# Performance work log

Hardware: AMD Instinct MI355X
Metric: run time of the kernel (lower is better)

## Reference

```python
import jax, jax.numpy as jnp
import numpy as np

EMBED = 512
H = 8
HD = EMBED // H           # 64
NUM_CLS = 4
WIN = 32                  # one-sided window radius
DIL = 1
WLEN = 2 * WIN + 1        # 65
CTX = NUM_CLS + WLEN      # 69
PATCH_LEN = 8192
B = 1
S = NUM_CLS + PATCH_LEN
THETA = 10000.0
COORD_HIGH = 100000.0
NEG = -1e30


def _rotate_half(x):
    # [..., x1, x2, ...] -> [..., -x2, x1, ...]
    x1 = x[..., 0::2]
    x2 = x[..., 1::2]
    return jnp.stack([-x2, x1], axis=-1).reshape(x.shape)


def _rope2d(x, coords):
    # x: (B,H,L,HD), coords: (B,L,2)
    half = HD // 2
    inv_freq = 1.0 / (THETA ** (jnp.arange(0, half, 2, dtype=jnp.float32) / half))  # (half//2,)
    xy = coords / COORD_HIGH
    fx = xy[..., 0][..., None] * inv_freq   # (B,L,half//2)
    fy = xy[..., 1][..., None] * inv_freq
    fx = jnp.repeat(fx, 2, axis=-1)         # (B,L,half)
    fy = jnp.repeat(fy, 2, axis=-1)
    freqs = jnp.concatenate([fx, fy], axis=-1)[:, None]  # (B,1,L,HD)
    return x * jnp.cos(freqs) + _rotate_half(x) * jnp.sin(freqs)


def setup_inputs() -> dict:
    key = jax.random.key(0)
    k1, k2, k3, k4, k5, k6 = jax.random.split(key, 6)
    x = jax.random.normal(k1, (B, S, EMBED), dtype=jnp.float32)
    coords = jax.random.uniform(k2, (B, PATCH_LEN, 2), dtype=jnp.float32) * COORD_HIGH
    sc = 1.0 / np.sqrt(EMBED)
    w_qkv = jax.random.normal(k3, (3 * EMBED, EMBED), dtype=jnp.float32) * sc
    b_qkv = jax.random.normal(k4, (3 * EMBED,), dtype=jnp.float32) * 0.02
    w_out = jax.random.normal(k5, (EMBED, EMBED), dtype=jnp.float32) * sc
    b_out = jax.random.normal(k6, (EMBED,), dtype=jnp.float32) * 0.02
    return {"x": x, "coords": coords, "w_qkv": w_qkv, "b_qkv": b_qkv,
            "w_out": w_out, "b_out": b_out}


def _forward(x, coords, w_qkv, b_qkv, w_out, b_out):
    Bb, seq_len, _ = x.shape
    qkv = x @ w_qkv.T + b_qkv                       # (B,S,3E)
    qkv = qkv.reshape(Bb, seq_len, 3, H, HD)
    qkv = jnp.transpose(qkv, (2, 0, 3, 1, 4))       # (3,B,H,S,HD)
    q, k, v = qkv[0], qkv[1], qkv[2]
    q_cls, k_cls, v_cls = q[:, :, :NUM_CLS], k[:, :, :NUM_CLS], v[:, :, :NUM_CLS]
    q_p, k_p, v_p = q[:, :, NUM_CLS:], k[:, :, NUM_CLS:], v[:, :, NUM_CLS:]

    q_p = _rope2d(q_p, coords)
    k_p = _rope2d(k_p, coords)
    k_all = jnp.concatenate([k_cls, k_p], axis=2)
    v_all = v

    scale = 1.0 / np.sqrt(HD)

    # --- global CLS attention: CLS queries attend to everything ---
    cls_scores = jnp.einsum('bhqd,bhkd->bhqk', q_cls, k_all) * scale
    cls_probs = jax.nn.softmax(cls_scores, axis=-1)
    cls_out = jnp.einsum('bhqk,bhkd->bhqd', cls_probs, v_all)

    # --- windowed patch attention: patch i -> [CLS | patches i-W..i+W (dilated)] ---
    L = PATCH_LEN
    pad = WIN * DIL
    k_pad = jnp.pad(k_p, ((0, 0), (0, 0), (pad, pad), (0, 0)))
    v_pad = jnp.pad(v_p, ((0, 0), (0, 0), (pad, pad), (0, 0)))
    gather_idx = jnp.arange(L)[:, None] + jnp.arange(WLEN)[None, :] * DIL  # (L,WLEN)
    k_win = k_pad[:, :, gather_idx]   # (B,H,L,WLEN,HD)
    v_win = v_pad[:, :, gather_idx]

    s_cls = jnp.einsum('bhld,bhcd->bhlc', q_p, k_cls) * scale     # (B,H,L,NUM_CLS)
    s_win = jnp.einsum('bhld,bhlwd->bhlw', q_p, k_win) * scale    # (B,H,L,WLEN)

    pos = jnp.arange(L)[:, None] + (jnp.arange(WLEN)[None, :] - WIN) * DIL
    in_bounds = (pos >= 0) & (pos < L)                            # (L,WLEN)
    s_win = jnp.where(in_bounds[None, None], s_win, NEG)

    scores = jnp.concatenate([s_cls, s_win], axis=-1)             # (B,H,L,CTX)
    probs = jax.nn.softmax(scores, axis=-1)
    p_cls, p_win = probs[..., :NUM_CLS], probs[..., NUM_CLS:]
    patch_out = (jnp.einsum('bhlc,bhcd->bhld', p_cls, v_cls)
                 + jnp.einsum('bhlw,bhlwd->bhld', p_win, v_win))

    out = jnp.concatenate([cls_out, patch_out], axis=2)           # (B,H,S,HD)
    out = jnp.transpose(out, (0, 2, 1, 3)).reshape(Bb, seq_len, EMBED)
    return out @ w_out.T + b_out


def reference(x, coords, w_qkv, b_qkv, w_out, b_out):
    return _forward(x, coords, w_qkv, b_qkv, w_out, b_out)
```

## Files before the change

kernel.cpp:

```cpp
#include <hip/hip_runtime.h>
#include <math.h>

#define EMBED 512
#define NHEAD 8
#define HD 64
#define NUM_CLS 4
#define WIN 32
#define WLEN 65
#define PATCH_LEN 8192
#define S_TOT 8196
#define QKV_LD 1536
#define VT_LD 8200

typedef short bf16x8 __attribute__((ext_vector_type(8)));
typedef float f32x4 __attribute__((ext_vector_type(4)));

__device__ __forceinline__ unsigned short f2bf(float f) {
    unsigned u = __float_as_uint(f);
    return (unsigned short)((u + 0x7fffu + ((u >> 16) & 1u)) >> 16);
}
__device__ __forceinline__ float bf2f(unsigned short v) {
    return __uint_as_float((unsigned)v << 16);
}
__device__ __forceinline__ void gll16(const unsigned short* g, unsigned short* l) {
    __builtin_amdgcn_global_load_lds((const __attribute__((address_space(1))) void*)g,
                                     (__attribute__((address_space(3))) void*)l, 16, 0, 0);
}

__global__ __launch_bounds__(256) void cast_all(const float* __restrict__ x,
                                                const float* __restrict__ wq,
                                                const float* __restrict__ wo,
                                                unsigned short* __restrict__ xb,
                                                unsigned short* __restrict__ wqb,
                                                unsigned short* __restrict__ wob)
{
    const int n1 = S_TOT * EMBED;
    const int n2 = 3 * EMBED * EMBED;
    const int n3 = EMBED * EMBED;
    const int i = (blockIdx.x * 256 + threadIdx.x) * 4;
    const float* src;
    unsigned short* dst;
    int j;
    if (i < n1)           { src = x;  dst = xb;  j = i; }
    else if (i < n1 + n2) { src = wq; dst = wqb; j = i - n1; }
    else if (i < n1 + n2 + n3) { src = wo; dst = wob; j = i - n1 - n2; }
    else return;
    const float4 v = *(const float4*)(src + j);
    ushort4 o;
    o.x = f2bf(v.x); o.y = f2bf(v.y); o.z = f2bf(v.z); o.w = f2bf(v.w);
    *(ushort4*)(dst + j) = o;
}

#define EXW 136
__global__ __launch_bounds__(256) void gemm_qkv(const unsigned short* __restrict__ A,
                                                const unsigned short* __restrict__ B,
                                                const float* __restrict__ bias,
                                                unsigned short* __restrict__ C,
                                                const float* __restrict__ coords,
                                                unsigned short* __restrict__ vT)
{
    const int M = S_TOT, N = 3 * EMBED, K = EMBED;
    __shared__ __align__(16) unsigned short As[2][128 * 32];
    __shared__ __align__(16) unsigned short Bs[2][128 * 32];
    __shared__ __align__(16) unsigned short EX[64 * EXW];
    const int tid = threadIdx.x;
    const int lane = tid & 63, w = tid >> 6;
    const int bn = blockIdx.x, bm = blockIdx.y;

    const int ar0 = tid >> 2;
    const int col8 = (tid & 3) * 8;
    int gm0 = bm * 128 + ar0;       if (gm0 >= M) gm0 = M - 1;
    int gm1 = bm * 128 + ar0 + 64;  if (gm1 >= M) gm1 = M - 1;
    const unsigned short* pa0 = A + (size_t)gm0 * K + col8;
    const unsigned short* pa1 = A + (size_t)gm1 * K + col8;
    const unsigned short* pb0 = B + (size_t)(bn * 128 + ar0) * K + col8;
    const unsigned short* pb1 = B + (size_t)(bn * 128 + ar0 + 64) * K + col8;

    const int wr = (w & 1) * 64;
    const int wc = (w >> 1) * 64;
    const int fr = lane & 15;
    const int fk = (lane >> 4) * 8;

    f32x4 acc[4][4];
#pragma unroll
    for (int mi = 0; mi < 4; ++mi)
#pragma unroll
        for (int ni = 0; ni < 4; ++ni) acc[mi][ni] = (f32x4)0.f;

    gll16(pa0, As[0] + tid * 8);
    gll16(pa1, As[0] + (tid + 256) * 8);
    gll16(pb0, Bs[0] + tid * 8);
    gll16(pb1, Bs[0] + (tid + 256) * 8);

    for (int it = 0; it < 16; ++it) {
        __syncthreads();
        if (it + 1 < 16) {
            const int k0 = (it + 1) * 32;
            const int nb = (it + 1) & 1;
            gll16(pa0 + k0, As[nb] + tid * 8);
            gll16(pa1 + k0, As[nb] + (tid + 256) * 8);
            gll16(pb0 + k0, Bs[nb] + tid * 8);
            gll16(pb1 + k0, Bs[nb] + (tid + 256) * 8);
        }
        const int cb = it & 1;
        bf16x8 af[4], bf[4];
#pragma unroll
        for (int mi = 0; mi < 4; ++mi)
            af[mi] = *(const bf16x8*)(As[cb] + (wr + mi * 16 + fr) * 32 + fk);
#pragma unroll
        for (int ni = 0; ni < 4; ++ni)
            bf[ni] = *(const bf16x8*)(Bs[cb] + (wc + ni * 16 + fr) * 32 + fk);
#pragma unroll
        for (int mi = 0; mi < 4; ++mi)
#pragma unroll
            for (int ni = 0; ni < 4; ++ni)
                acc[mi][ni] = __builtin_amdgcn_mfma_f32_16x16x32_bf16(af[mi], bf[ni], acc[mi][ni], 0, 0, 0);
    }

    const int ccol = bn * 128 + wc + fr;

    if (bn < 8) {
        ushort2* rt = (ushort2*)EX;
        for (int idx = tid; idx < 4096; idx += 256) {
            const int rr = idx >> 5, pr = idx & 31;
            int l = bm * 128 + rr - NUM_CLS;
            l = l < 0 ? 0 : (l > PATCH_LEN - 1 ? PATCH_LEN - 1 : l);
            const float cxy = coords[l * 2 + (pr >> 4)] * 1e-5f;
            const float f = cxy * __expf(-(float)(pr & 15) * 0.5756462732485114f);
            float sn, cs;
            __sincosf(f, &sn, &cs);
            ushort2 e; e.x = f2bf(cs); e.y = f2bf(sn);
            rt[idx] = e;
        }
        __syncthreads();

        unsigned pv[4][4][2];
#pragma unroll
        for (int mi = 0; mi < 4; ++mi) {
#pragma unroll
            for (int r = 0; r < 4; ++r) {
                const int rloc = wr + mi * 16 + (lane >> 4) * 4 + r;
                const int row = bm * 128 + rloc;
                const bool patch = (row >= NUM_CLS) && (row < M);
#pragma unroll
                for (int ni = 0; ni < 4; ++ni) {
                    const int col = ccol + ni * 16;
                    const float biased = acc[mi][ni][r] + bias[col];
                    const float prt = __shfl_xor(biased, 1);
                    float outv = biased;
                    if (patch) {
                        const ushort2 e = rt[rloc * 32 + ((col & 63) >> 1)];
                        const float cs = bf2f(e.x), sn = bf2f(e.y);
                        outv = (col & 1) ? (biased * cs + prt * sn)
                                         : (biased * cs - prt * sn);
                    }
                    const unsigned us = f2bf(outv);
                    if (r & 1) pv[mi][ni][r >> 1] |= us << 16;
                    else       pv[mi][ni][r >> 1] = us;
                }
            }
        }
        for (int p = 0; p < 2; ++p) {
            __syncthreads();
            if ((w & 1) == p) {
#pragma unroll
                for (int mi = 0; mi < 4; ++mi) {
#pragma unroll
                    for (int r = 0; r < 4; ++r) {
                        const int rl = mi * 16 + (lane >> 4) * 4 + r;
#pragma unroll
                        for (int ni = 0; ni < 4; ++ni) {
                            const unsigned pw = pv[mi][ni][r >> 1];
                            EX[rl * EXW + wc + fr + ni * 16] =
                                (unsigned short)((r & 1) ? (pw >> 16) : (pw & 0xffff));
                        }
                    }
                }
            }
            __syncthreads();
#pragma unroll
            for (int i = 0; i < 4; ++i) {
                const int idx = tid + 256 * i;
                const int rowl = idx >> 4, ch = idx & 15;
                const int grow = bm * 128 + p * 64 + rowl;
                if (grow < M)
                    *(bf16x8*)(C + (size_t)grow * N + bn * 128 + ch * 8) =
                        *(const bf16x8*)(EX + rowl * EXW + ch * 8);
            }
        }
    } else {
        const int dbase = (bn - 8) * 128;
#pragma unroll
        for (int mi = 0; mi < 4; ++mi) {
            const int rbase = bm * 128 + wr + mi * 16 + (lane >> 4) * 4;
#pragma unroll
            for (int ni = 0; ni < 4; ++ni) {
                const int col = ccol + ni * 16;
#pragma unroll
                for (int r = 0; r < 4; ++r) {
                    const int row = rbase + r;
                    if (row < M)
                        C[(size_t)row * N + col] = f2bf(acc[mi][ni][r] + bias[col]);
                }
            }
        }
        for (int p = 0; p < 2; ++p) {
            __syncthreads();
            if ((w >> 1) == p) {
#pragma unroll
                for (int mi = 0; mi < 4; ++mi) {
                    const int tok0 = wr + mi * 16 + (lane >> 4) * 4;
                    const int rw = bm * 128 + tok0;
#pragma unroll
                    for (int ni = 0; ni < 4; ++ni) {
                        const int col = ccol + ni * 16;
                        const int dloc = fr + 16 * ni;
                        ushort4 o;
                        o.x = (rw + 0 < M) ? f2bf(acc[mi][ni][0] + bias[col]) : (unsigned short)0;
                        o.y = (rw + 1 < M) ? f2bf(acc[mi][ni][1] + bias[col]) : (unsigned short)0;
                        o.z = (rw + 2 < M) ? f2bf(acc[mi][ni][2] + bias[col]) : (unsigned short)0;
                        o.w = (rw + 3 < M) ? f2bf(acc[mi][ni][3] + bias[col]) : (unsigned short)0;
                        *(ushort4*)(EX + dloc * EXW + tok0) = o;
                    }
                }
            }
            __syncthreads();
            const int d = tid >> 2;
            const int tch = (tid & 3) * 32;
            const int gtok = bm * 128 + tch;
            unsigned short* dst = vT + (size_t)(dbase + p * 64 + d) * VT_LD + gtok;
            const unsigned short* srcl = EX + d * EXW + tch;
            if (gtok + 32 <= VT_LD) {
#pragma unroll
                for (int c2 = 0; c2 < 32; c2 += 8)
                    *(bf16x8*)(dst + c2) = *(const bf16x8*)(srcl + c2);
            } else {
                for (int c2 = 0; c2 < 32; ++c2)
                    if (gtok + c2 < VT_LD) dst[c2] = srcl[c2];
            }
        }
    }
}

__global__ __launch_bounds__(256) void gemm_out(const unsigned short* __restrict__ A,
                                                const unsigned short* __restrict__ B,
                                                const float* __restrict__ bias,
                                                float* __restrict__ C)
{
    const int M = S_TOT, N = EMBED, K = EMBED;
    __shared__ __align__(16) unsigned short As[2][64 * 32];
    __shared__ __align__(16) unsigned short Bs[2][128 * 32];
    const int tid = threadIdx.x;
    const int lane = tid & 63, w = tid >> 6;
    const int bn = blockIdx.x, bm = blockIdx.y;

    const int ar0 = tid >> 2;
    const int col8 = (tid & 3) * 8;
    int gm0 = bm * 64 + ar0;  if (gm0 >= M) gm0 = M - 1;
    const unsigned short* pa0 = A + (size_t)gm0 * K + col8;
    const unsigned short* pb0 = B + (size_t)(bn * 128 + ar0) * K + col8;
    const unsigned short* pb1 = B + (size_t)(bn * 128 + ar0 + 64) * K + col8;

    const int wr = (w & 1) * 32;
    const int wc = (w >> 1) * 64;
    const int fr = lane & 15;
    const int fk = (lane >> 4) * 8;

    f32x4 acc[2][4];
#pragma unroll
    for (int mi = 0; mi < 2; ++mi)
#pragma unroll
        for (int ni = 0; ni < 4; ++ni) acc[mi][ni] = (f32x4)0.f;

    gll16(pa0, As[0] + tid * 8);
    gll16(pb0, Bs[0] + tid * 8);
    gll16(pb1, Bs[0] + (tid + 256) * 8);

    for (int it = 0; it < 16; ++it) {
        __syncthreads();
        if (it + 1 < 16) {
            const int k0 = (it + 1) * 32;
            const int nb = (it + 1) & 1;
            gll16(pa0 + k0, As[nb] + tid * 8);
            gll16(pb0 + k0, Bs[nb] + tid * 8);
            gll16(pb1 + k0, Bs[nb] + (tid + 256) * 8);
        }
        const int cb = it & 1;
        bf16x8 af[2], bf[4];
#pragma unroll
        for (int mi = 0; mi < 2; ++mi)
            af[mi] = *(const bf16x8*)(As[cb] + (wr + mi * 16 + fr) * 32 + fk);
#pragma unroll
        for (int ni = 0; ni < 4; ++ni)
            bf[ni] = *(const bf16x8*)(Bs[cb] + (wc + ni * 16 + fr) * 32 + fk);
#pragma unroll
        for (int mi = 0; mi < 2; ++mi)
#pragma unroll
            for (int ni = 0; ni < 4; ++ni)
                acc[mi][ni] = __builtin_amdgcn_mfma_f32_16x16x32_bf16(af[mi], bf[ni], acc[mi][ni], 0, 0, 0);
    }

    const int ccol = bn * 128 + wc + fr;
#pragma unroll
    for (int mi = 0; mi < 2; ++mi) {
        const int rbase = bm * 64 + wr + mi * 16 + (lane >> 4) * 4;
#pragma unroll
        for (int r = 0; r < 4; ++r) {
            const int row = rbase + r;
            if (row < M) {
#pragma unroll
                for (int ni = 0; ni < 4; ++ni)
                    C[(size_t)row * N + ccol + ni * 16] = acc[mi][ni][r] + bias[ccol + ni * 16];
            }
        }
    }
}

#define CCH 128
#define NCHUNK ((S_TOT + CCH - 1) / CCH)
#define PSTRIDE 68

__global__ __launch_bounds__(256) void cls_attn_partial(const unsigned short* __restrict__ qkv,
                                                        float* __restrict__ part)
{
    const int h = blockIdx.x;
    const int c = blockIdx.y;
    const int tid = threadIdx.x;
    const int base = c * CCH;

    __shared__ float qs[4][64];
    __shared__ __align__(16) unsigned short Kl[128 * 64];
    __shared__ float sc[4][CCH];
    __shared__ float ored[4][4][64];
    __shared__ float ml[4][2];

    {
        const int qi = tid >> 6, d = tid & 63;
        qs[qi][d] = bf2f(qkv[(size_t)qi * QKV_LD + h * HD + d]);
    }
    for (int i = tid; i < 1024; i += 256) {
        const int kr = i >> 3;
        const int dc = (i & 7) ^ (kr & 7);
        int j = base + kr; if (j > S_TOT - 1) j = S_TOT - 1;
        gll16(qkv + (size_t)j * QKV_LD + EMBED + h * HD + dc * 8, Kl + i * 8);
    }
    __syncthreads();

    {
        const int jj = tid & 127;
        const int qp = (tid >> 7) * 2;
        const int j = base + jj;
        float s0 = -INFINITY, s1 = -INFINITY;
        if (j < S_TOT) {
            float a0 = 0.f, a1 = 0.f;
#pragma unroll
            for (int cch = 0; cch < 8; ++cch) {
                const int slot = cch ^ (jj & 7);
                const bf16x8 kv8 = *(const bf16x8*)(Kl + jj * 64 + slot * 8);
#pragma unroll
                for (int u = 0; u < 8; ++u) {
                    const float kf = bf2f((unsigned short)kv8[u]);
                    a0 += qs[qp + 0][cch * 8 + u] * kf;
                    a1 += qs[qp + 1][cch * 8 + u] * kf;
                }
            }
            s0 = a0 * 0.125f; s1 = a1 * 0.125f;
        }
        sc[qp + 0][jj] = s0;
        sc[qp + 1][jj] = s1;
    }
    __syncthreads();

    const int w = tid >> 6, lane = tid & 63;
    {
        float m = fmaxf(sc[w][lane], sc[w][lane + 64]);
#pragma unroll
        for (int off = 32; off > 0; off >>= 1) m = fmaxf(m, __shfl_xor(m, off, 64));
        const float e0 = expf(sc[w][lane] - m);
        const float e1 = expf(sc[w][lane + 64] - m);
        sc[w][lane] = e0; sc[w][lane + 64] = e1;
        float lsum = e0 + e1;
#pragma unroll
        for (int off = 32; off > 0; off >>= 1) lsum += __shfl_xor(lsum, off, 64);
        if (lane == 0) { ml[w][0] = m; ml[w][1] = lsum; }
    }
    __syncthreads();

    {
        const int g = w, d = lane;
        float a0 = 0.f, a1 = 0.f, a2 = 0.f, a3 = 0.f;
        for (int jj = g; jj < CCH; jj += 4) {
            const int j = base + jj;
            if (j >= S_TOT) break;
            const float vv = bf2f(qkv[(size_t)j * QKV_LD + 2 * EMBED + h * HD + d]);
            a0 += sc[0][jj] * vv; a1 += sc[1][jj] * vv;
            a2 += sc[2][jj] * vv; a3 += sc[3][jj] * vv;
        }
        ored[g][0][d] = a0; ored[g][1][d] = a1; ored[g][2][d] = a2; ored[g][3][d] = a3;
    }
    __syncthreads();

    {
        const int qi = tid >> 6, d = tid & 63;
        const float o = ored[0][qi][d] + ored[1][qi][d] + ored[2][qi][d] + ored[3][qi][d];
        float* pb = part + ((size_t)(h * NCHUNK + c) * 4 + qi) * PSTRIDE;
        pb[d] = o;
        if (d == 0) { pb[64] = ml[qi][0]; pb[65] = ml[qi][1]; }
    }
}

__global__ __launch_bounds__(256) void cls_attn_combine(const float* __restrict__ part,
                                                        unsigned short* __restrict__ attn)
{
    const int h = blockIdx.x;
    const int qi = threadIdx.x >> 6, d = threadIdx.x & 63;
    float M = -INFINITY;
    for (int c = 0; c < NCHUNK; ++c)
        M = fmaxf(M, part[((size_t)(h * NCHUNK + c) * 4 + qi) * PSTRIDE + 64]);
    float acc = 0.f, L = 0.f;
    for (int c = 0; c < NCHUNK; ++c) {
        const float* pb = part + ((size_t)(h * NCHUNK + c) * 4 + qi) * PSTRIDE;
        const float s = expf(pb[64] - M);
        acc += s * pb[d];
        L   += s * pb[65];
    }
    attn[(size_t)qi * EMBED + h * HD + d] = f2bf(acc / L);
}

#define SW 116
#define PW 136

__global__ __launch_bounds__(256) void patch_attn_mfma(
    const unsigned short* __restrict__ qkv,
    const unsigned short* __restrict__ vT,
    unsigned short* __restrict__ attnb)
{
    const int l0 = blockIdx.x * 32;
    const int h = blockIdx.y;
    const int tid = threadIdx.x;
    const int lane = tid & 63, w = tid >> 6;

    __shared__ __align__(16) unsigned short Qs[32 * 64];
    __shared__ __align__(16) unsigned short Ks[112 * 64];
    __shared__ __align__(16) unsigned short Vt[64 * 128];
    __shared__ __align__(16) float Sm[32 * SW];

    {
        const int i = tid;
        const int t = i >> 3;
        const int dcl = (i & 7) ^ (t & 7);
        gll16(qkv + (size_t)(NUM_CLS + l0 + t) * QKV_LD + h * HD + dcl * 8, Qs + i * 8);
    }
    for (int i = tid; i < 896; i += 256) {
        const int c = i >> 3;
        const int dcl = (i & 7) ^ (c & 7);
        int tok = (c >= 104 && c < 108) ? (c - 104) : (l0 - 32 + c);
        tok = tok < 0 ? 0 : (tok > S_TOT - 1 ? S_TOT - 1 : tok);
        gll16(qkv + (size_t)tok * QKV_LD + EMBED + h * HD + dcl * 8, Ks + i * 8);
    }
    for (int i = tid; i < 1024; i += 256) {
        const int d = i >> 4;
        const int kcl = (i & 15) ^ (d & 15);
        const int c0 = kcl * 8;
        int tokb = (c0 == 104) ? 0 : (l0 - 32 + c0);
        tokb = tokb < 0 ? 0 : (tokb > 8192 ? 8192 : tokb);
        gll16(vT + (size_t)(h * HD + d) * VT_LD + tokb, Vt + i * 8);
    }
    __syncthreads();

    bf16x8 qf[2][2];
#pragma unroll
    for (int mt = 0; mt < 2; ++mt)
#pragma unroll
        for (int ks = 0; ks < 2; ++ks) {
            const int row = mt * 16 + (lane & 15);
            const int dc = (ks * 4 + (lane >> 4)) ^ (row & 7);
            qf[mt][ks] = *(const bf16x8*)(Qs + row * 64 + dc * 8);
        }
    for (int idx = w; idx < 14; idx += 4) {
        const int mt = idx & 1, nt = idx >> 1;
        f32x4 acc = (f32x4)0.f;
#pragma unroll
        for (int ks = 0; ks < 2; ++ks) {
            const int kr = nt * 16 + (lane & 15);
            const int dc = (ks * 4 + (lane >> 4)) ^ (kr & 7);
            const bf16x8 kf = *(const bf16x8*)(Ks + kr * 64 + dc * 8);
            acc = __builtin_amdgcn_mfma_f32_16x16x32_bf16(qf[mt][ks], kf, acc, 0, 0, 0);
        }
        const int col = nt * 16 + (lane & 15);
        const int r0 = mt * 16 + (lane >> 4) * 4;
#pragma unroll
        for (int r = 0; r < 4; ++r) Sm[(r0 + r) * SW + col] = acc[r];
    }
    __syncthreads();

    {
        const int t = tid >> 3, lq = tid & 7;
        float e[14];
        float m = -INFINITY;
#pragma unroll
        for (int j = 0; j < 14; ++j) {
            const int c = lq + 8 * j;
            bool valid;
            if (c >= 104) valid = (c < 108);
            else {
                const int r = c - 4;
                const int pos = l0 - 32 + r;
                valid = (c >= 4) && (c < 100) && (r >= t) && (r <= t + 64) &&
                        (pos >= 0) && (pos < PATCH_LEN);
            }
            e[j] = valid ? Sm[t * SW + c] * 0.125f : -INFINITY;
            m = fmaxf(m, e[j]);
        }
#pragma unroll
        for (int off = 1; off < 8; off <<= 1) m = fmaxf(m, __shfl_xor(m, off, 64));
        float sum = 0.f;
#pragma unroll
        for (int j = 0; j < 14; ++j) { e[j] = expf(e[j] - m); sum += e[j]; }
#pragma unroll
        for (int off = 1; off < 8; off <<= 1) sum += __shfl_xor(sum, off, 64);
        const float inv = 1.f / sum;
        __syncthreads();
        unsigned short* P = (unsigned short*)Sm;
#pragma unroll
        for (int j = 0; j < 14; ++j) P[t * PW + lq + 8 * j] = f2bf(e[j] * inv);
        ushort2 z; z.x = 0; z.y = 0;
        *(ushort2*)(P + (tid >> 3) * PW + 112 + (tid & 7) * 2) = z;
    }
    __syncthreads();

    {
        const unsigned short* P = (const unsigned short*)Sm;
        const int mt = w & 1;
        bf16x8 pf[4];
#pragma unroll
        for (int ks = 0; ks < 4; ++ks) {
            const int row = mt * 16 + (lane & 15);
            pf[ks] = *(const bf16x8*)(P + row * PW + ks * 32 + (lane >> 4) * 8);
        }
#pragma unroll
        for (int nn = 0; nn < 2; ++nn) {
            const int nt = (w >> 1) + nn * 2;
            f32x4 acc = (f32x4)0.f;
#pragma unroll
            for (int ks = 0; ks < 4; ++ks) {
                const int d = nt * 16 + (lane & 15);
                const int kc = (ks * 4 + (lane >> 4)) ^ (d & 15);
                const bf16x8 vf = *(const bf16x8*)(Vt + d * 128 + kc * 8);
                acc = __builtin_amdgcn_mfma_f32_16x16x32_bf16(pf[ks], vf, acc, 0, 0, 0);
            }
            const int dcol = nt * 16 + (lane & 15);
            const int r0 = mt * 16 + (lane >> 4) * 4;
#pragma unroll
            for (int r = 0; r < 4; ++r)
                attnb[(size_t)(NUM_CLS + l0 + r0 + r) * EMBED + h * HD + dcol] = f2bf(acc[r]);
        }
    }
}

extern "C" void kernel_launch(void* const* d_in, const int* in_sizes, int n_in,
                              void* d_out, int out_size, void* d_ws, size_t ws_size,
                              hipStream_t stream)
{
    const float* x      = (const float*)d_in[0];
    const float* coords = (const float*)d_in[1];
    const float* w_qkv  = (const float*)d_in[2];
    const float* b_qkv  = (const float*)d_in[3];
    const float* w_out  = (const float*)d_in[4];
    const float* b_out  = (const float*)d_in[5];
    float* out = (float*)d_out;

    char* p = (char*)d_ws;
    unsigned short* qkv   = (unsigned short*)p;  p += (size_t)S_TOT * QKV_LD * 2;
    unsigned short* vT    = (unsigned short*)p;  p += (size_t)EMBED * VT_LD * 2;
    unsigned short* attnb = (unsigned short*)p;  p += (size_t)S_TOT * EMBED * 2;
    float*          part  = (float*)p;           p += (size_t)NHEAD * NCHUNK * 4 * PSTRIDE * 4;
    unsigned short* wob   = (unsigned short*)p;  p += (size_t)EMBED * EMBED * 2;
    unsigned short* xb    = (unsigned short*)p;  p += (size_t)S_TOT * EMBED * 2;
    unsigned short* wqb   = (unsigned short*)p;


    {
        const int total = S_TOT * EMBED + 3 * EMBED * EMBED + EMBED * EMBED;
        cast_all<<<(total / 4 + 255) / 256, 256, 0, stream>>>(x, w_qkv, w_out, xb, wqb, wob);
    }

    gemm_qkv<<<dim3(12, 65), 256, 0, stream>>>(xb, wqb, b_qkv, qkv, coords, vT);

    cls_attn_partial<<<dim3(NHEAD, NCHUNK), 256, 0, stream>>>(qkv, part);
    cls_attn_combine<<<NHEAD, 256, 0, stream>>>(part, attnb);

    patch_attn_mfma<<<dim3(PATCH_LEN / 32, NHEAD), 256, 0, stream>>>(qkv, vT, attnb);

    gemm_out<<<dim3(4, 129), 256, 0, stream>>>(attnb, wob, b_out, out);
}
```

Measured before the change: 194.0 us.

## Alias QKV GEMM LDS buffers and remap blocks for XCD-local row reuse

The QKV GEMM's double-buffered A/B tiles and the epilogue staging buffer now share one aliased LDS array, which cuts shared memory per block and may allow more resident blocks. A barrier is added after the main loop so the epilogue can reuse that space safely. The 2D grid becomes a 1D grid of 864 blocks, remapped so each XCD handles whole row-tiles across all 12 column tiles, aiming to improve L2 reuse of the A rows. Blocks past the 65 row tiles exit early, which wastes a few launches.

Result: faster. 185.0 us (-4.7%).

```diff
diff --git a/kernel.cpp b/kernel.cpp
--- a/kernel.cpp
+++ b/kernel.cpp
@@ -60,12 +60,16 @@
                                                 unsigned short* __restrict__ vT)
 {
     const int M = S_TOT, N = 3 * EMBED, K = EMBED;
-    __shared__ __align__(16) unsigned short As[2][128 * 32];
-    __shared__ __align__(16) unsigned short Bs[2][128 * 32];
-    __shared__ __align__(16) unsigned short EX[64 * EXW];
+    __shared__ __align__(16) unsigned short SMEM[16384];
+    unsigned short* EX = SMEM;
+
     const int tid = threadIdx.x;
     const int lane = tid & 63, w = tid >> 6;
-    const int bn = blockIdx.x, bm = blockIdx.y;
+    const int xcd = blockIdx.x & 7;
+    const int s = blockIdx.x >> 3;
+    const int bm = xcd + 8 * (s / 12);
+    const int bn = s % 12;
+    if (bm >= 65) return;
 
     const int ar0 = tid >> 2;
     const int col8 = (tid & 3) * 8;
@@ -87,35 +91,37 @@
 #pragma unroll
         for (int ni = 0; ni < 4; ++ni) acc[mi][ni] = (f32x4)0.f;
 
-    gll16(pa0, As[0] + tid * 8);
-    gll16(pa1, As[0] + (tid + 256) * 8);
-    gll16(pb0, Bs[0] + tid * 8);
-    gll16(pb1, Bs[0] + (tid + 256) * 8);
+    gll16(pa0, SMEM + tid * 8);
+    gll16(pa1, SMEM + (tid + 256) * 8);
+    gll16(pb0, SMEM + 8192 + tid * 8);
+    gll16(pb1, SMEM + 8192 + (tid + 256) * 8);
 
     for (int it = 0; it < 16; ++it) {
         __syncthreads();
         if (it + 1 < 16) {
             const int k0 = (it + 1) * 32;
-            const int nb = (it + 1) & 1;
-            gll16(pa0 + k0, As[nb] + tid * 8);
-            gll16(pa1 + k0, As[nb] + (tid + 256) * 8);
-            gll16(pb0 + k0, Bs[nb] + tid * 8);
-            gll16(pb1 + k0, Bs[nb] + (tid + 256) * 8);
-        }
-        const int cb = it & 1;
+            const int off = ((it + 1) & 1) * 4096;
+            gll16(pa0 + k0, SMEM + off + tid * 8);
+            gll16(pa1 + k0, SMEM + off + (tid + 256) * 8);
+            gll16(pb0 + k0, SMEM + 8192 + off + tid * 8);
+            gll16(pb1 + k0, SMEM + 8192 + off + (tid + 256) * 8);
+        }
+        const unsigned short* Asb = SMEM + (it & 1) * 4096;
+        const unsigned short* Bsb = SMEM + 8192 + (it & 1) * 4096;
         bf16x8 af[4], bf[4];
 #pragma unroll
         for (int mi = 0; mi < 4; ++mi)
-            af[mi] = *(const bf16x8*)(As[cb] + (wr + mi * 16 + fr) * 32 + fk);
+            af[mi] = *(const bf16x8*)(Asb + (wr + mi * 16 + fr) * 32 + fk);
 #pragma unroll
         for (int ni = 0; ni < 4; ++ni)
-            bf[ni] = *(const bf16x8*)(Bs[cb] + (wc + ni * 16 + fr) * 32 + fk);
+            bf[ni] = *(const bf16x8*)(Bsb + (wc + ni * 16 + fr) * 32 + fk);
 #pragma unroll
         for (int mi = 0; mi < 4; ++mi)
 #pragma unroll
             for (int ni = 0; ni < 4; ++ni)
                 acc[mi][ni] = __builtin_amdgcn_mfma_f32_16x16x32_bf16(af[mi], bf[ni], acc[mi][ni], 0, 0, 0);
     }
+    __syncthreads();
 
     const int ccol = bn * 128 + wc + fr;
 
@@ -585,7 +591,7 @@
         cast_all<<<(total / 4 + 255) / 256, 256, 0, stream>>>(x, w_qkv, w_out, xb, wqb, wob);
     }
 
-    gemm_qkv<<<dim3(12, 65), 256, 0, stream>>>(xb, wqb, b_qkv, qkv, coords, vT);
+    gemm_qkv<<<864, 256, 0, stream>>>(xb, wqb, b_qkv, qkv, coords, vT);
 
     cls_attn_partial<<<dim3(NHEAD, NCHUNK), 256, 0, stream>>>(qkv, part);
     cls_attn_combine<<<NHEAD, 256, 0, stream>>>(part, attnb);
```
